# Optimization experiments

Hardware: AMD Instinct MI355X
Metric: run time of the kernel (lower is better)

The kernel has to match this reference:

```python
import jax, jax.numpy as jnp
import numpy as np
import math

B, S, H, DK = 16, 4096, 16, 64
DM = H * DK          # 1024, d_model
QD = 1024            # q_d_model
KVD = 1024           # kv_d_model
MASK_P = 0.85        # randbool probability


def setup_inputs() -> dict:
    key = jax.random.key(0)
    ks = jax.random.split(key, 12)
    s = 0.02
    return {
        "q": jax.random.normal(ks[0], (B, 1, QD), jnp.float32),
        "k": jax.random.normal(ks[1], (B, S, KVD), jnp.float32),
        "v": jax.random.normal(ks[2], (B, S, KVD), jnp.float32),
        "Wq": jax.random.normal(ks[3], (QD, DM), jnp.float32) * s,
        "bq": jnp.zeros((DM,), jnp.float32),
        "Wk": jax.random.normal(ks[4], (KVD, DM), jnp.float32) * s,
        "bk": jnp.zeros((DM,), jnp.float32),
        "Wv": jax.random.normal(ks[5], (KVD, DM), jnp.float32) * s,
        "bv": jnp.zeros((DM,), jnp.float32),
        "Wo": jax.random.normal(ks[6], (DM, QD), jnp.float32) * s,
        "bo": jnp.zeros((QD,), jnp.float32),
        # randbool(shape, p=0.85): True where rand < p -> score zeroed
        "maskfill": jax.random.uniform(ks[7], (B, H, 1, S)) < MASK_P,
    }


def reference(q, k, v, Wq, bq, Wk, bk, Wv, bv, Wo, bo, maskfill):
    bs = q.shape[0]
    # projections -> [B, L, H, DK] -> [B, H, L, DK]
    qh = (q @ Wq + bq).reshape(bs, -1, H, DK).transpose(0, 2, 1, 3)  # [B,H,1,DK]
    kh = (k @ Wk + bk).reshape(bs, -1, H, DK).transpose(0, 2, 1, 3)  # [B,H,S,DK]
    vh = (v @ Wv + bv).reshape(bs, -1, H, DK).transpose(0, 2, 1, 3)  # [B,H,S,DK]

    scores1 = jnp.einsum("bhqd,bhkd->bhqk", qh, kh) / math.sqrt(DK)  # [B,H,1,S]

    # plain path (dropout = identity in eval)
    attn = jax.nn.softmax(scores1, axis=-1)
    out_h = jnp.einsum("bhqk,bhkd->bhqd", attn, vh)                  # [B,H,1,DK]

    # masked path: zero-fill (not -inf) masked raw scores, then softmax
    masked_scores = jnp.where(maskfill, 0.0, scores1)
    mattn = jax.nn.softmax(masked_scores, axis=-1)
    mout_h = jnp.einsum("bhqk,bhkd->bhqd", mattn, vh)

    concat = out_h.transpose(0, 2, 1, 3).reshape(bs, DM)
    mconcat = mout_h.transpose(0, 2, 1, 3).reshape(bs, DM)
    output = concat @ Wo + bo
    masked_output = mconcat @ Wo + bo
    return (output, masked_output)
```

## Files before the change

### kernel.cpp

```cpp
#include <hip/hip_runtime.h>
#include <stdint.h>

#define NB 16
#define NS 4096
#define NH 16
#define NC 1024

#define OFF_QHP   0u
#define OFF_QK    262144u
#define OFF_QB    524288u
#define OFF_SP    524608u
#define OFF_ATT   540992u
#define OFF_CTXP  2638144u
#define OFF_CON   11026752u

__global__ __launch_bounds__(128) void k_qh(
    const float* __restrict__ q, const float* __restrict__ Wq, float* __restrict__ qhp)
{
    __shared__ float qs[64*16];
    int dz = blockIdx.x, cs = blockIdx.y;
    int tid = threadIdx.x;
    int d = dz*128 + tid;
#pragma unroll
    for (int j = 0; j < 2; ++j) {
        int idx = j*128 + tid;
        int b = idx >> 4, c4 = (idx & 15) << 2;
        float4 t = *(const float4*)(q + (size_t)b*NC + cs*64 + c4);
        qs[(c4+0)*16 + b] = t.x; qs[(c4+1)*16 + b] = t.y;
        qs[(c4+2)*16 + b] = t.z; qs[(c4+3)*16 + b] = t.w;
    }
    __syncthreads();
    float acc[16];
#pragma unroll
    for (int b = 0; b < 16; ++b) acc[b] = 0.f;
#pragma unroll 4
    for (int c = 0; c < 64; ++c) {
        float w = Wq[(size_t)(cs*64 + c)*NC + d];
        const float4* qr = (const float4*)(qs + c*16);
        float4 q0 = qr[0], q1 = qr[1], q2 = qr[2], q3 = qr[3];
        acc[0]  = fmaf(w, q0.x, acc[0]);  acc[1]  = fmaf(w, q0.y, acc[1]);
        acc[2]  = fmaf(w, q0.z, acc[2]);  acc[3]  = fmaf(w, q0.w, acc[3]);
        acc[4]  = fmaf(w, q1.x, acc[4]);  acc[5]  = fmaf(w, q1.y, acc[5]);
        acc[6]  = fmaf(w, q1.z, acc[6]);  acc[7]  = fmaf(w, q1.w, acc[7]);
        acc[8]  = fmaf(w, q2.x, acc[8]);  acc[9]  = fmaf(w, q2.y, acc[9]);
        acc[10] = fmaf(w, q2.z, acc[10]); acc[11] = fmaf(w, q2.w, acc[11]);
        acc[12] = fmaf(w, q3.x, acc[12]); acc[13] = fmaf(w, q3.y, acc[13]);
        acc[14] = fmaf(w, q3.z, acc[14]); acc[15] = fmaf(w, q3.w, acc[15]);
    }
#pragma unroll
    for (int b = 0; b < 16; ++b) qhp[((size_t)cs*16 + b)*NC + d] = acc[b];
}

__global__ __launch_bounds__(128) void k_qk(
    const float* __restrict__ qhp, const float* __restrict__ bq,
    const float* __restrict__ Wk, const float* __restrict__ bk,
    float* __restrict__ qko, float* __restrict__ qbv)
{
    int h = blockIdx.x;
    int c = blockIdx.y*128 + threadIdx.x;
    __shared__ float qs[16*64];
    for (int j = 0; j < 8; ++j) {
        int idx = j*128 + threadIdx.x;
        int b = idx >> 6, dd = idx & 63;
        float a = bq[h*64 + dd];
#pragma unroll
        for (int cs = 0; cs < 16; ++cs) a += qhp[((size_t)cs*16 + b)*NC + h*64 + dd];
        qs[idx] = a;
    }
    __syncthreads();
    const float* wr = Wk + (size_t)c*NC + h*64;
    float acc[16];
#pragma unroll
    for (int b = 0; b < 16; ++b) acc[b] = 0.f;
#pragma unroll 4
    for (int d = 0; d < 64; ++d) {
        float w = wr[d];
#pragma unroll
        for (int b = 0; b < 16; ++b) acc[b] = fmaf(qs[b*64 + d], w, acc[b]);
    }
#pragma unroll
    for (int b = 0; b < 16; ++b) qko[((size_t)b*NH + h)*NC + c] = acc[b];
    if (blockIdx.y == 0 && threadIdx.x < 16) {
        int b = threadIdx.x; float a = 0.f;
        for (int d = 0; d < 64; ++d) a = fmaf(qs[b*64 + d], bk[h*64 + d], a);
        qbv[b*NH + h] = a;
    }
}

#define QTS 20
#define SCOMP(BUF, W)                                                          \
    _Pragma("unroll")                                                          \
    for (int j = 0; j < 4; ++j) {                                              \
        const float* qp = qt + ((W)*16 + ph*4 + j)*QTS + hg*4;                 \
        float4 qv = *(const float4*)qp;                                        \
        _Pragma("unroll")                                                      \
        for (int i = 0; i < 8; ++i) {                                          \
            float kc = (j == 0) ? BUF[i].x : (j == 1) ? BUF[i].y               \
                     : (j == 2) ? BUF[i].z : BUF[i].w;                         \
            acc[i][0] = fmaf(kc, qv.x, acc[i][0]);                             \
            acc[i][1] = fmaf(kc, qv.y, acc[i][1]);                             \
            acc[i][2] = fmaf(kc, qv.z, acc[i][2]);                             \
            acc[i][3] = fmaf(kc, qv.w, acc[i][3]);                             \
        }                                                                      \
    }
__global__ __launch_bounds__(256) void k_scoresI2(
    const float* __restrict__ kk, const float* __restrict__ qkm,
    const float* __restrict__ qbv, const void* __restrict__ mask,
    float* __restrict__ att, float* __restrict__ Sp)
{
    __shared__ float qt[512*QTS];
    __shared__ float red[4][2][16];
    int sb = blockIdx.x, b = blockIdx.y;
    int tid = threadIdx.x;
    int ph = tid & 3, hg = (tid >> 2) & 3, rg = tid >> 4;
    int srow = sb*128 + rg*8;

    int fl;
    {
        const uint4* mw = (const uint4*)mask;
        unsigned f = 0u, g = 0u;
#pragma unroll
        for (int j = 0; j < 8; ++j) {
            uint4 m4 = mw[j];
            f |= (m4.x == 0x3F800000u) | (m4.y == 0x3F800000u)
               | (m4.z == 0x3F800000u) | (m4.w == 0x3F800000u);
            g |= ((m4.x > 1u) & (m4.x != 0x3F800000u))
               | ((m4.y > 1u) & (m4.y != 0x3F800000u))
               | ((m4.z > 1u) & (m4.z != 0x3F800000u))
               | ((m4.w > 1u) & (m4.w != 0x3F800000u));
        }
        fl = f ? 2 : (g ? 1 : 0);
    }

    const float* kr = kk + ((size_t)b*NS + srow)*NC + ph*4;
    float acc[8][4];
#pragma unroll
    for (int i = 0; i < 8; ++i)
#pragma unroll
        for (int j = 0; j < 4; ++j) acc[i][j] = 0.f;

    for (int cz = 0; cz < 2; ++cz) {
        __syncthreads();
#pragma unroll
        for (int j = 0; j < 32; ++j) {
            int idx = j*256 + tid;
            int h = idx >> 9, c = idx & 511;
            qt[c*QTS + h] = qkm[((size_t)b*NH + h)*NC + cz*512 + c];
        }
        __syncthreads();
        const float* kc0 = kr + cz*512;
        float4 A[8], B[8], T[8];
#pragma unroll
        for (int i = 0; i < 8; ++i) A[i] = *(const float4*)(kc0 + i*NC);
#pragma unroll
        for (int i = 0; i < 8; ++i) B[i] = *(const float4*)(kc0 + i*NC + 16);
        for (int w = 0; w < 32; w += 2) {
            if (w + 2 < 32) {
#pragma unroll
                for (int i = 0; i < 8; ++i)
                    T[i] = *(const float4*)(kc0 + i*NC + (w+2)*16);
            }
            SCOMP(A, w);
            if (w + 3 < 32) {
#pragma unroll
                for (int i = 0; i < 8; ++i)
                    A[i] = *(const float4*)(kc0 + i*NC + (w+3)*16);
            }
            SCOMP(B, (w+1));
#pragma unroll
            for (int i = 0; i < 8; ++i) { B[i] = A[i]; A[i] = T[i]; }
        }
    }
#pragma unroll
    for (int i = 0; i < 8; ++i)
#pragma unroll
        for (int j = 0; j < 4; ++j) {
            acc[i][j] += __shfl_xor(acc[i][j], 1, 64);
            acc[i][j] += __shfl_xor(acc[i][j], 2, 64);
        }
    float d0[4], d1[4];
    if (ph == 0) {
#pragma unroll
        for (int j = 0; j < 4; ++j) { d0[j] = acc[0][j]; d1[j] = acc[1][j]; }
    } else if (ph == 1) {
#pragma unroll
        for (int j = 0; j < 4; ++j) { d0[j] = acc[2][j]; d1[j] = acc[3][j]; }
    } else if (ph == 2) {
#pragma unroll
        for (int j = 0; j < 4; ++j) { d0[j] = acc[4][j]; d1[j] = acc[5][j]; }
    } else {
#pragma unroll
        for (int j = 0; j < 4; ++j) { d0[j] = acc[6][j]; d1[j] = acc[7][j]; }
    }
    int sA = srow + 2*ph, sB = sA + 1;
    unsigned mA = 0, mB = 0;
    if (fl == 1) {
        const uint8_t* mp = (const uint8_t*)mask + (size_t)(b*NH + hg*4)*NS;
#pragma unroll
        for (int j = 0; j < 4; ++j) {
            if (mp[(size_t)j*NS + sA]) mA |= (1u << j);
            if (mp[(size_t)j*NS + sB]) mB |= (1u << j);
        }
    } else if (fl == 2) {
        const float* mp = (const float*)mask + (size_t)(b*NH + hg*4)*NS;
#pragma unroll
        for (int j = 0; j < 4; ++j) {
            if (mp[(size_t)j*NS + sA] != 0.f) mA |= (1u << j);
            if (mp[(size_t)j*NS + sB] != 0.f) mB |= (1u << j);
        }
    } else {
        const int* mp = (const int*)mask + (size_t)(b*NH + hg*4)*NS;
#pragma unroll
        for (int j = 0; j < 4; ++j) {
            if (mp[(size_t)j*NS + sA]) mA |= (1u << j);
            if (mp[(size_t)j*NS + sB]) mB |= (1u << j);
        }
    }
    float p0a[4], p1a[4], p0b[4], p1b[4], r0[4], r1[4];
#pragma unroll
    for (int j = 0; j < 4; ++j) {
        float qb = qbv[b*NH + hg*4 + j];
        float va = (d0[j] + qb) * 0.125f;
        float vb = (d1[j] + qb) * 0.125f;
        p0a[j] = __expf(va);  p1a[j] = (mA >> j & 1u) ? 1.0f : p0a[j];
        p0b[j] = __expf(vb);  p1b[j] = (mB >> j & 1u) ? 1.0f : p0b[j];
        r0[j] = p0a[j] + p0b[j];
        r1[j] = p1a[j] + p1b[j];
    }
    float* aA = att + ((size_t)b*NS + sA)*32 + hg*4;
    float* aB = att + ((size_t)b*NS + sB)*32 + hg*4;
    *(float4*)(aA)      = make_float4(p0a[0], p0a[1], p0a[2], p0a[3]);
    *(float4*)(aA + 16) = make_float4(p1a[0], p1a[1], p1a[2], p1a[3]);
    *(float4*)(aB)      = make_float4(p0b[0], p0b[1], p0b[2], p0b[3]);
    *(float4*)(aB + 16) = make_float4(p1b[0], p1b[1], p1b[2], p1b[3]);

#pragma unroll
    for (int j = 0; j < 4; ++j) {
        r0[j] += __shfl_xor(r0[j], 1, 64);  r1[j] += __shfl_xor(r1[j], 1, 64);
        r0[j] += __shfl_xor(r0[j], 2, 64);  r1[j] += __shfl_xor(r1[j], 2, 64);
        r0[j] += __shfl_xor(r0[j], 16, 64); r1[j] += __shfl_xor(r1[j], 16, 64);
        r0[j] += __shfl_xor(r0[j], 32, 64); r1[j] += __shfl_xor(r1[j], 32, 64);
    }
    int wv = tid >> 6;
    if ((tid & 51) == 0) {
#pragma unroll
        for (int j = 0; j < 4; ++j) {
            red[wv][0][hg*4 + j] = r0[j];
            red[wv][1][hg*4 + j] = r1[j];
        }
    }
    __syncthreads();
    if (tid < 32) {
        int pa = tid >> 4, h = tid & 15;
        Sp[((size_t)b*32 + sb)*32 + tid] =
            red[0][pa][h] + red[1][pa][h] + red[2][pa][h] + red[3][pa][h];
    }
}

__global__ __launch_bounds__(256,2) void k_ctx(
    const float* __restrict__ v, const float* __restrict__ att, float* __restrict__ ctxp)
{
    __shared__ float al[64*32];
    __shared__ float buf[8192];
    int b = blockIdx.x & 15, ss = blockIdx.x >> 4;
    int cz = blockIdx.y;
    int tid = threadIdx.x, ct = tid & 63, rg = tid >> 6;
    int s1 = ss * 256;
    float acc[32][4];
#pragma unroll
    for (int i = 0; i < 32; ++i)
#pragma unroll
        for (int j = 0; j < 4; ++j) acc[i][j] = 0.f;

    for (int c0 = 0; c0 < 256; c0 += 64) {
        __syncthreads();
#pragma unroll
        for (int jj = 0; jj < 2; ++jj) {
            int idx = jj*256 + tid;
            ((float4*)al)[idx] = ((const float4*)(att + ((size_t)b*NS + s1 + c0)*32))[idx];
        }
        __syncthreads();
        for (int it = 0; it < 16; ++it) {
            int rl = c0 + it*4 + rg;
            float4 vv = *(const float4*)(v + ((size_t)b*NS + s1 + rl)*NC + cz*256 + ct*4);
            const float4* ar = (const float4*)(al + (it*4 + rg)*32);
#pragma unroll
            for (int u = 0; u < 8; ++u) {
                float4 aw = ar[u];
                acc[u*4+0][0] = fmaf(aw.x, vv.x, acc[u*4+0][0]);
                acc[u*4+0][1] = fmaf(aw.x, vv.y, acc[u*4+0][1]);
                acc[u*4+0][2] = fmaf(aw.x, vv.z, acc[u*4+0][2]);
                acc[u*4+0][3] = fmaf(aw.x, vv.w, acc[u*4+0][3]);
                acc[u*4+1][0] = fmaf(aw.y, vv.x, acc[u*4+1][0]);
                acc[u*4+1][1] = fmaf(aw.y, vv.y, acc[u*4+1][1]);
                acc[u*4+1][2] = fmaf(aw.y, vv.z, acc[u*4+1][2]);
                acc[u*4+1][3] = fmaf(aw.y, vv.w, acc[u*4+1][3]);
                acc[u*4+2][0] = fmaf(aw.z, vv.x, acc[u*4+2][0]);
                acc[u*4+2][1] = fmaf(aw.z, vv.y, acc[u*4+2][1]);
                acc[u*4+2][2] = fmaf(aw.z, vv.z, acc[u*4+2][2]);
                acc[u*4+2][3] = fmaf(aw.z, vv.w, acc[u*4+2][3]);
                acc[u*4+3][0] = fmaf(aw.w, vv.x, acc[u*4+3][0]);
                acc[u*4+3][1] = fmaf(aw.w, vv.y, acc[u*4+3][1]);
                acc[u*4+3][2] = fmaf(aw.w, vv.z, acc[u*4+3][2]);
                acc[u*4+3][3] = fmaf(aw.w, vv.w, acc[u*4+3][3]);
            }
        }
    }
    for (int pr = 0; pr < 4; ++pr) {
        __syncthreads();
#pragma unroll
        for (int u = 0; u < 8; ++u) {
            int ph = pr*8 + u;
            float4 t; t.x = acc[ph][0]; t.y = acc[ph][1]; t.z = acc[ph][2]; t.w = acc[ph][3];
            ((float4*)buf)[(rg*8 + u)*64 + ct] = t;
        }
        __syncthreads();
#pragma unroll
        for (int kx = 0; kx < 2; ++kx) {
            int i = kx*256 + tid;
            int u2 = i >> 6, c2 = i & 63;
            float4 s = ((float4*)buf)[(size_t)(0*8 + u2)*64 + c2];
#pragma unroll
            for (int r2 = 1; r2 < 4; ++r2) {
                float4 t = ((float4*)buf)[(size_t)(r2*8 + u2)*64 + c2];
                s.x += t.x; s.y += t.y; s.z += t.z; s.w += t.w;
            }
            int ph = pr*8 + u2, p = ph >> 4, h = ph & 15;
            *(float4*)(ctxp + ((((size_t)ss*2 + p)*NB + b)*NH + h)*NC + cz*256 + c2*4) = s;
        }
    }
}

__global__ __launch_bounds__(256) void k_outhN(
    const float* __restrict__ ctxp, const float* __restrict__ Sp,
    const float* __restrict__ Wv, const float* __restrict__ bv,
    float* __restrict__ con)
{
    int b = blockIdx.y, p = blockIdx.z;
    int dx = blockIdx.x;
    int d = dx*256 + threadIdx.x;
    int h0 = dx*4;
    __shared__ float cl[4*NC];
    float Sinv[4];
#pragma unroll
    for (int j = 0; j < 4; ++j) {
        float a = 0.f;
        for (int sb = 0; sb < 32; ++sb)
            a += Sp[((size_t)b*32 + sb)*32 + p*16 + h0 + j];
        Sinv[j] = 1.f / a;
    }
#pragma unroll
    for (int hh = 0; hh < 4; ++hh) {
        for (int cc = threadIdx.x; cc < NC; cc += 256) {
            float a = 0.f;
#pragma unroll
            for (int ss = 0; ss < 16; ++ss)
                a += ctxp[((((size_t)ss*2 + p)*NB + b)*NH + h0 + hh)*NC + cc];
            cl[hh*NC + cc] = a * Sinv[hh];
        }
    }
    __syncthreads();
    const float* c2 = cl + ((threadIdx.x >> 6) << 10);
    float a0=0.f,a1=0.f,a2=0.f,a3=0.f;
    for (int c = 0; c < NC; c += 4) {
        a0 = fmaf(c2[c+0], Wv[(size_t)(c+0)*NC + d], a0);
        a1 = fmaf(c2[c+1], Wv[(size_t)(c+1)*NC + d], a1);
        a2 = fmaf(c2[c+2], Wv[(size_t)(c+2)*NC + d], a2);
        a3 = fmaf(c2[c+3], Wv[(size_t)(c+3)*NC + d], a3);
    }
    con[((size_t)p*NB + b)*NC + d] = (a0+a1)+(a2+a3) + bv[d];
}

__global__ __launch_bounds__(256) void k_out(
    const float* __restrict__ con, const float* __restrict__ Wo,
    const float* __restrict__ bo, float* __restrict__ out)
{
    int b = blockIdx.y, p = blockIdx.z;
    int o = blockIdx.x*256 + threadIdx.x;
    __shared__ float cl[NC];
    for (int i = threadIdx.x; i < NC; i += 256)
        cl[i] = con[((size_t)p*NB + b)*NC + i];
    __syncthreads();
    float a0=0.f,a1=0.f,a2=0.f,a3=0.f;
    for (int m = 0; m < NC; m += 4) {
        a0 = fmaf(cl[m+0], Wo[(size_t)(m+0)*NC + o], a0);
        a1 = fmaf(cl[m+1], Wo[(size_t)(m+1)*NC + o], a1);
        a2 = fmaf(cl[m+2], Wo[(size_t)(m+2)*NC + o], a2);
        a3 = fmaf(cl[m+3], Wo[(size_t)(m+3)*NC + o], a3);
    }
    out[(size_t)p*NB*NC + (size_t)b*NC + o] = (a0+a1)+(a2+a3) + bo[o];
}

extern "C" void kernel_launch(void* const* d_in, const int* in_sizes, int n_in,
                              void* d_out, int out_size, void* d_ws, size_t ws_size,
                              hipStream_t stream)
{
    (void)in_sizes; (void)n_in; (void)out_size; (void)ws_size;
    const float* q  = (const float*)d_in[0];
    const float* k  = (const float*)d_in[1];
    const float* v  = (const float*)d_in[2];
    const float* Wq = (const float*)d_in[3];
    const float* bq = (const float*)d_in[4];
    const float* Wk = (const float*)d_in[5];
    const float* bk = (const float*)d_in[6];
    const float* Wv = (const float*)d_in[7];
    const float* bv = (const float*)d_in[8];
    const float* Wo = (const float*)d_in[9];
    const float* bo = (const float*)d_in[10];
    const void*  mk = d_in[11];

    float* ws   = (float*)d_ws;
    float* qhp  = ws + OFF_QHP;
    float* qkv  = ws + OFF_QK;
    float* qbv  = ws + OFF_QB;
    float* Sp   = ws + OFF_SP;
    float* att  = ws + OFF_ATT;
    float* ctxp = ws + OFF_CTXP;
    float* con  = ws + OFF_CON;
    float* out  = (float*)d_out;

    k_qh<<<dim3(8, 16), 128, 0, stream>>>(q, Wq, qhp);
    k_qk<<<dim3(16, 8), 128, 0, stream>>>(qhp, bq, Wk, bk, qkv, qbv);
    k_scoresI2<<<dim3(32, 16), 256, 0, stream>>>(k, qkv, qbv, mk, att, Sp);
    k_ctx<<<dim3(256, 4), 256, 0, stream>>>(v, att, ctxp);
    k_outhN<<<dim3(4, NB, 2), 256, 0, stream>>>(ctxp, Sp, Wv, bv, con);
    k_out<<<dim3(4, NB, 2), 256, 0, stream>>>(con, Wo, bo, out);
}
```

Before: 309.8 us.

## Fuse score and context kernels, keep attention weights in LDS

Merges the score/exp kernel and the attention-times-V kernel into one 512-thread block per 256-row chunk. Exponentiated weights for both masked and unmasked paths go to swizzled shared memory instead of a global att buffer, then each block reduces its V slab directly into per-chunk ctx partials. This removes the global att write/read round trip and one launch. In exchange the grid shrinks to 256 large blocks with heavy register use and more LDS, lowering occupancy, and the score and V phases now run back to back inside each block. The K prefetch is also reduced from two tiles ahead to one.

```diff
diff --git a/kernel.cpp b/kernel.cpp
--- a/kernel.cpp
+++ b/kernel.cpp
@@ -10,9 +10,8 @@
 #define OFF_QK    262144u
 #define OFF_QB    524288u
 #define OFF_SP    524608u
-#define OFF_ATT   540992u
-#define OFF_CTXP  2638144u
-#define OFF_CON   11026752u
+#define OFF_CTXP  532800u
+#define OFF_CON   8921408u
 
 __global__ __launch_bounds__(128) void k_qh(
     const float* __restrict__ q, const float* __restrict__ Wq, float* __restrict__ qhp)
@@ -103,17 +102,18 @@
             acc[i][3] = fmaf(kc, qv.w, acc[i][3]);                             \
         }                                                                      \
     }
-__global__ __launch_bounds__(256) void k_scoresI2(
-    const float* __restrict__ kk, const float* __restrict__ qkm,
-    const float* __restrict__ qbv, const void* __restrict__ mask,
-    float* __restrict__ att, float* __restrict__ Sp)
+__global__ __launch_bounds__(512) void k_att(
+    const float* __restrict__ kk, const float* __restrict__ vv,
+    const float* __restrict__ qkm, const float* __restrict__ qbv,
+    const void* __restrict__ mask, float* __restrict__ ctxp, float* __restrict__ Sp)
 {
     __shared__ float qt[512*QTS];
-    __shared__ float red[4][2][16];
+    __shared__ float attl[256*32];
+    __shared__ float red[8][2][16];
     int sb = blockIdx.x, b = blockIdx.y;
     int tid = threadIdx.x;
     int ph = tid & 3, hg = (tid >> 2) & 3, rg = tid >> 4;
-    int srow = sb*128 + rg*8;
+    int srow = sb*256 + rg*8;
 
     int fl;
     {
@@ -142,33 +142,25 @@
     for (int cz = 0; cz < 2; ++cz) {
         __syncthreads();
 #pragma unroll
-        for (int j = 0; j < 32; ++j) {
-            int idx = j*256 + tid;
+        for (int j = 0; j < 16; ++j) {
+            int idx = j*512 + tid;
             int h = idx >> 9, c = idx & 511;
             qt[c*QTS + h] = qkm[((size_t)b*NH + h)*NC + cz*512 + c];
         }
         __syncthreads();
         const float* kc0 = kr + cz*512;
-        float4 A[8], B[8], T[8];
-#pragma unroll
-        for (int i = 0; i < 8; ++i) A[i] = *(const float4*)(kc0 + i*NC);
-#pragma unroll
-        for (int i = 0; i < 8; ++i) B[i] = *(const float4*)(kc0 + i*NC + 16);
-        for (int w = 0; w < 32; w += 2) {
-            if (w + 2 < 32) {
+        float4 kv[8], kn[8];
+#pragma unroll
+        for (int i = 0; i < 8; ++i) kv[i] = *(const float4*)(kc0 + i*NC);
+        for (int w = 0; w < 32; ++w) {
+            if (w < 31) {
 #pragma unroll
                 for (int i = 0; i < 8; ++i)
-                    T[i] = *(const float4*)(kc0 + i*NC + (w+2)*16);
+                    kn[i] = *(const float4*)(kc0 + i*NC + (w+1)*16);
             }
-            SCOMP(A, w);
-            if (w + 3 < 32) {
-#pragma unroll
-                for (int i = 0; i < 8; ++i)
-                    A[i] = *(const float4*)(kc0 + i*NC + (w+3)*16);
-            }
-            SCOMP(B, (w+1));
-#pragma unroll
-            for (int i = 0; i < 8; ++i) { B[i] = A[i]; A[i] = T[i]; }
+            SCOMP(kv, w);
+#pragma unroll
+            for (int i = 0; i < 8; ++i) kv[i] = kn[i];
         }
     }
 #pragma unroll
@@ -192,7 +184,8 @@
 #pragma unroll
         for (int j = 0; j < 4; ++j) { d0[j] = acc[6][j]; d1[j] = acc[7][j]; }
     }
-    int sA = srow + 2*ph, sB = sA + 1;
+    int lA = rg*8 + 2*ph, lB = lA + 1;
+    int sA = sb*256 + lA, sB = sA + 1;
     unsigned mA = 0, mB = 0;
     if (fl == 1) {
         const uint8_t* mp = (const uint8_t*)mask + (size_t)(b*NH + hg*4)*NS;
@@ -227,13 +220,13 @@
         r0[j] = p0a[j] + p0b[j];
         r1[j] = p1a[j] + p1b[j];
     }
-    float* aA = att + ((size_t)b*NS + sA)*32 + hg*4;
-    float* aB = att + ((size_t)b*NS + sB)*32 + hg*4;
-    *(float4*)(aA)      = make_float4(p0a[0], p0a[1], p0a[2], p0a[3]);
-    *(float4*)(aA + 16) = make_float4(p1a[0], p1a[1], p1a[2], p1a[3]);
-    *(float4*)(aB)      = make_float4(p0b[0], p0b[1], p0b[2], p0b[3]);
-    *(float4*)(aB + 16) = make_float4(p1b[0], p1b[1], p1b[2], p1b[3]);
-
+    {
+        int swA = (lA & 7) << 2, swB = (lB & 7) << 2;
+        *(float4*)(attl + lA*32 + ((hg*4) ^ swA))        = make_float4(p0a[0], p0a[1], p0a[2], p0a[3]);
+        *(float4*)(attl + lA*32 + ((16 + hg*4) ^ swA))   = make_float4(p1a[0], p1a[1], p1a[2], p1a[3]);
+        *(float4*)(attl + lB*32 + ((hg*4) ^ swB))        = make_float4(p0b[0], p0b[1], p0b[2], p0b[3]);
+        *(float4*)(attl + lB*32 + ((16 + hg*4) ^ swB))   = make_float4(p1b[0], p1b[1], p1b[2], p1b[3]);
+    }
 #pragma unroll
     for (int j = 0; j < 4; ++j) {
         r0[j] += __shfl_xor(r0[j], 1, 64);  r1[j] += __shfl_xor(r1[j], 1, 64);
@@ -252,81 +245,67 @@
     __syncthreads();
     if (tid < 32) {
         int pa = tid >> 4, h = tid & 15;
-        Sp[((size_t)b*32 + sb)*32 + tid] =
-            red[0][pa][h] + red[1][pa][h] + red[2][pa][h] + red[3][pa][h];
-    }
-}
-
-__global__ __launch_bounds__(256,2) void k_ctx(
-    const float* __restrict__ v, const float* __restrict__ att, float* __restrict__ ctxp)
-{
-    __shared__ float al[64*32];
-    __shared__ float buf[8192];
-    int b = blockIdx.x & 15, ss = blockIdx.x >> 4;
-    int cz = blockIdx.y;
-    int tid = threadIdx.x, ct = tid & 63, rg = tid >> 6;
-    int s1 = ss * 256;
-    float acc[32][4];
-#pragma unroll
-    for (int i = 0; i < 32; ++i)
-#pragma unroll
-        for (int j = 0; j < 4; ++j) acc[i][j] = 0.f;
-
-    for (int c0 = 0; c0 < 256; c0 += 64) {
-        __syncthreads();
-#pragma unroll
-        for (int jj = 0; jj < 2; ++jj) {
-            int idx = jj*256 + tid;
-            ((float4*)al)[idx] = ((const float4*)(att + ((size_t)b*NS + s1 + c0)*32))[idx];
-        }
-        __syncthreads();
-        for (int it = 0; it < 16; ++it) {
-            int rl = c0 + it*4 + rg;
-            float4 vv = *(const float4*)(v + ((size_t)b*NS + s1 + rl)*NC + cz*256 + ct*4);
-            const float4* ar = (const float4*)(al + (it*4 + rg)*32);
-#pragma unroll
-            for (int u = 0; u < 8; ++u) {
-                float4 aw = ar[u];
-                acc[u*4+0][0] = fmaf(aw.x, vv.x, acc[u*4+0][0]);
-                acc[u*4+0][1] = fmaf(aw.x, vv.y, acc[u*4+0][1]);
-                acc[u*4+0][2] = fmaf(aw.x, vv.z, acc[u*4+0][2]);
-                acc[u*4+0][3] = fmaf(aw.x, vv.w, acc[u*4+0][3]);
-                acc[u*4+1][0] = fmaf(aw.y, vv.x, acc[u*4+1][0]);
-                acc[u*4+1][1] = fmaf(aw.y, vv.y, acc[u*4+1][1]);
-                acc[u*4+1][2] = fmaf(aw.y, vv.z, acc[u*4+1][2]);
-                acc[u*4+1][3] = fmaf(aw.y, vv.w, acc[u*4+1][3]);
-                acc[u*4+2][0] = fmaf(aw.z, vv.x, acc[u*4+2][0]);
-                acc[u*4+2][1] = fmaf(aw.z, vv.y, acc[u*4+2][1]);
-                acc[u*4+2][2] = fmaf(aw.z, vv.z, acc[u*4+2][2]);
-                acc[u*4+2][3] = fmaf(aw.z, vv.w, acc[u*4+2][3]);
-                acc[u*4+3][0] = fmaf(aw.w, vv.x, acc[u*4+3][0]);
-                acc[u*4+3][1] = fmaf(aw.w, vv.y, acc[u*4+3][1]);
-                acc[u*4+3][2] = fmaf(aw.w, vv.z, acc[u*4+3][2]);
-                acc[u*4+3][3] = fmaf(aw.w, vv.w, acc[u*4+3][3]);
-            }
-        }
-    }
+        float a = 0.f;
+#pragma unroll
+        for (int w8 = 0; w8 < 8; ++w8) a += red[w8][pa][h];
+        Sp[((size_t)b*16 + sb)*32 + tid] = a;
+    }
+
+    int cq = tid & 255, half = tid >> 8;
+    float cacc[32][4];
+#pragma unroll
+    for (int u = 0; u < 32; ++u)
+#pragma unroll
+        for (int j = 0; j < 4; ++j) cacc[u][j] = 0.f;
+    const float* vb = vv + ((size_t)b*NS + sb*256 + half*128)*NC + cq*4;
+    for (int r = 0; r < 128; ++r) {
+        float4 vvv = *(const float4*)(vb + (size_t)r*NC);
+        int l = half*128 + r;
+        const float* ar = attl + l*32;
+        int lw = l & 7;
+#pragma unroll
+        for (int g = 0; g < 8; ++g) {
+            float4 aw = *(const float4*)(ar + ((g ^ lw) << 2));
+            cacc[g*4+0][0] = fmaf(aw.x, vvv.x, cacc[g*4+0][0]);
+            cacc[g*4+0][1] = fmaf(aw.x, vvv.y, cacc[g*4+0][1]);
+            cacc[g*4+0][2] = fmaf(aw.x, vvv.z, cacc[g*4+0][2]);
+            cacc[g*4+0][3] = fmaf(aw.x, vvv.w, cacc[g*4+0][3]);
+            cacc[g*4+1][0] = fmaf(aw.y, vvv.x, cacc[g*4+1][0]);
+            cacc[g*4+1][1] = fmaf(aw.y, vvv.y, cacc[g*4+1][1]);
+            cacc[g*4+1][2] = fmaf(aw.y, vvv.z, cacc[g*4+1][2]);
+            cacc[g*4+1][3] = fmaf(aw.y, vvv.w, cacc[g*4+1][3]);
+            cacc[g*4+2][0] = fmaf(aw.z, vvv.x, cacc[g*4+2][0]);
+            cacc[g*4+2][1] = fmaf(aw.z, vvv.y, cacc[g*4+2][1]);
+            cacc[g*4+2][2] = fmaf(aw.z, vvv.z, cacc[g*4+2][2]);
+            cacc[g*4+2][3] = fmaf(aw.z, vvv.w, cacc[g*4+2][3]);
+            cacc[g*4+3][0] = fmaf(aw.w, vvv.x, cacc[g*4+3][0]);
+            cacc[g*4+3][1] = fmaf(aw.w, vvv.y, cacc[g*4+3][1]);
+            cacc[g*4+3][2] = fmaf(aw.w, vvv.z, cacc[g*4+3][2]);
+            cacc[g*4+3][3] = fmaf(aw.w, vvv.w, cacc[g*4+3][3]);
+        }
+    }
+    float* buf = qt;
+#pragma unroll
     for (int pr = 0; pr < 4; ++pr) {
         __syncthreads();
-#pragma unroll
-        for (int u = 0; u < 8; ++u) {
-            int ph = pr*8 + u;
-            float4 t; t.x = acc[ph][0]; t.y = acc[ph][1]; t.z = acc[ph][2]; t.w = acc[ph][3];
-            ((float4*)buf)[(rg*8 + u)*64 + ct] = t;
+        if (half == 1) {
+#pragma unroll
+            for (int u = 0; u < 8; ++u)
+                *(float4*)(buf + (u*256 + cq)*4) =
+                    make_float4(cacc[pr*8+u][0], cacc[pr*8+u][1],
+                                cacc[pr*8+u][2], cacc[pr*8+u][3]);
         }
         __syncthreads();
-#pragma unroll
-        for (int kx = 0; kx < 2; ++kx) {
-            int i = kx*256 + tid;
-            int u2 = i >> 6, c2 = i & 63;
-            float4 s = ((float4*)buf)[(size_t)(0*8 + u2)*64 + c2];
-#pragma unroll
-            for (int r2 = 1; r2 < 4; ++r2) {
-                float4 t = ((float4*)buf)[(size_t)(r2*8 + u2)*64 + c2];
-                s.x += t.x; s.y += t.y; s.z += t.z; s.w += t.w;
+        if (half == 0) {
+#pragma unroll
+            for (int u = 0; u < 8; ++u) {
+                float4 t = *(const float4*)(buf + (u*256 + cq)*4);
+                int uph = pr*8 + u, p = uph >> 4, h = uph & 15;
+                float4 s;
+                s.x = cacc[pr*8+u][0] + t.x; s.y = cacc[pr*8+u][1] + t.y;
+                s.z = cacc[pr*8+u][2] + t.z; s.w = cacc[pr*8+u][3] + t.w;
+                *(float4*)(ctxp + ((((size_t)sb*2 + p)*NB + b)*NH + h)*NC + cq*4) = s;
             }
-            int ph = pr*8 + u2, p = ph >> 4, h = ph & 15;
-            *(float4*)(ctxp + ((((size_t)ss*2 + p)*NB + b)*NH + h)*NC + cz*256 + c2*4) = s;
         }
     }
 }
@@ -345,8 +324,8 @@
 #pragma unroll
     for (int j = 0; j < 4; ++j) {
         float a = 0.f;
-        for (int sb = 0; sb < 32; ++sb)
-            a += Sp[((size_t)b*32 + sb)*32 + p*16 + h0 + j];
+        for (int sb = 0; sb < 16; ++sb)
+            a += Sp[((size_t)b*16 + sb)*32 + p*16 + h0 + j];
         Sinv[j] = 1.f / a;
     }
 #pragma unroll
@@ -414,15 +393,13 @@
     float* qkv  = ws + OFF_QK;
     float* qbv  = ws + OFF_QB;
     float* Sp   = ws + OFF_SP;
-    float* att  = ws + OFF_ATT;
     float* ctxp = ws + OFF_CTXP;
     float* con  = ws + OFF_CON;
     float* out  = (float*)d_out;
 
     k_qh<<<dim3(8, 16), 128, 0, stream>>>(q, Wq, qhp);
     k_qk<<<dim3(16, 8), 128, 0, stream>>>(qhp, bq, Wk, bk, qkv, qbv);
-    k_scoresI2<<<dim3(32, 16), 256, 0, stream>>>(k, qkv, qbv, mk, att, Sp);
-    k_ctx<<<dim3(256, 4), 256, 0, stream>>>(v, att, ctxp);
+    k_att<<<dim3(16, 16), 512, 0, stream>>>(k, v, qkv, qbv, mk, ctxp, Sp);
     k_outhN<<<dim3(4, NB, 2), 256, 0, stream>>>(ctxp, Sp, Wv, bv, con);
     k_out<<<dim3(4, NB, 2), 256, 0, stream>>>(con, Wo, bo, out);
 }
```

Result: faster. 284.2 us (-8.2%).
